# Performance work log

Measured on AMD Instinct MI355X. Metric: run time of the kernel, lower is better.

The kernel has to match this reference:

```python
import jax, jax.numpy as jnp
import numpy as np

N = 262144      # total line-graph nodes (16 graphs x 16384)
E = 2097152     # total line-graph edges (avg degree 8)
F_IN = 8        # edge_attr feature dim
FEATURES_DIM = 64


def gcn_conv(x, src, dst, W, b, n):
    """PyG GCNConv: x' = D^{-1/2} (A+I) D^{-1/2} (x W) + b, deg from in-edges incl. self-loops."""
    x = x @ W
    loop = jnp.arange(n, dtype=src.dtype)
    si = jnp.concatenate([src, loop])
    di = jnp.concatenate([dst, loop])
    deg = jax.ops.segment_sum(jnp.ones(si.shape[0], dtype=x.dtype), di, num_segments=n)
    dinv = jnp.where(deg > 0, deg ** -0.5, 0.0)
    norm = dinv[si] * dinv[di]                      # [E+N]
    msg = x[si] * norm[:, None]                     # gather + scale
    return jax.ops.segment_sum(msg, di, num_segments=n) + b


def setup_inputs() -> dict:
    key = jax.random.key(0)
    ks = jax.random.split(key, 10)

    def lin(k, fan_in, fan_out):
        return jax.random.normal(k, (fan_in, fan_out), jnp.float32) * (1.0 / np.sqrt(fan_in))

    return {
        "x": jax.random.normal(ks[0], (N, F_IN), jnp.float32),
        "W1": lin(ks[1], F_IN, 16), "b1": jnp.zeros((16,), jnp.float32),
        "W2": lin(ks[2], 16, 32),   "b2": jnp.zeros((32,), jnp.float32),
        "W3": lin(ks[3], 32, 64),   "b3": jnp.zeros((64,), jnp.float32),
        "Wfc": lin(ks[4], 64, FEATURES_DIM), "bfc": jnp.zeros((FEATURES_DIM,), jnp.float32),
        "edge_index": jax.random.randint(ks[5], (2, E), 0, N, dtype=jnp.int32),
        "batch_size": 16,
    }


def reference(x, W1, b1, W2, b2, W3, b3, Wfc, bfc, edge_index, batch_size):
    src, dst = edge_index[0], edge_index[1]
    n = x.shape[0]
    h = jax.nn.relu(gcn_conv(x, src, dst, W1, b1, n))
    h = jax.nn.relu(gcn_conv(h, src, dst, W2, b2, n))
    h = jax.nn.relu(gcn_conv(h, src, dst, W3, b3, n))
    out = h @ Wfc + bfc
    return out.reshape(batch_size, -1, FEATURES_DIM)
```

## Files before the change

kernel.cpp:

```cpp
#include <hip/hip_runtime.h>
#include <hip/hip_bf16.h>


#define NB   256
#define NPB  1024
#define TILE 4096
#define SRCMASK 0x3FFFFu

typedef _Float16 half8 __attribute__((ext_vector_type(8)));
typedef float float4v __attribute__((ext_vector_type(4)));

__device__ __forceinline__ unsigned pkh(float a, float b) {
    unsigned short ua = __builtin_bit_cast(unsigned short, (_Float16)a);
    unsigned short ub = __builtin_bit_cast(unsigned short, (_Float16)b);
    return (unsigned)ua | ((unsigned)ub << 16);
}
__device__ __forceinline__ float h_lo(unsigned u) {
    return (float)__builtin_bit_cast(_Float16, (unsigned short)(u & 0xFFFFu));
}
__device__ __forceinline__ float h_hi(unsigned u) {
    return (float)__builtin_bit_cast(_Float16, (unsigned short)(u >> 16));
}

__global__ void hist_kernel(const int* __restrict__ dst, int* __restrict__ ghist,
                            int E, int shift) {
    __shared__ int h[NB];
    int tid = threadIdx.x;
    h[tid] = 0;
    __syncthreads();
    int base = blockIdx.x * TILE;
    int cnt = min(TILE, E - base);
    for (int i = tid; i < cnt; i += 256)
        atomicAdd(&h[dst[base + i] >> shift], 1);
    __syncthreads();
    int v = h[tid];
    if (v) atomicAdd(&ghist[tid], v);
}

__global__ void bscan_kernel(const int* __restrict__ ghist, int* __restrict__ bbase,
                             int* __restrict__ gcursor,
                             const float* __restrict__ W3, const float* __restrict__ Wf,
                             _Float16* __restrict__ w3f, _Float16* __restrict__ wff) {
    __shared__ int sh[NB];
    int tid = threadIdx.x;
    int v = ghist[tid];
    sh[tid] = v;
    __syncthreads();
    for (int o = 1; o < NB; o <<= 1) {
        int t = (tid >= o) ? sh[tid - o] : 0;
        __syncthreads();
        sh[tid] += t;
        __syncthreads();
    }
    int incl = sh[tid];
    bbase[tid] = incl - v;
    gcursor[tid] = incl - v;
    if (tid == NB - 1) bbase[NB] = incl;
    for (int i = tid; i < 32 * 64; i += NB) {
        int k = i >> 6, j = i & 63;
        w3f[(j >> 4) * 512 + (j & 15) * 32 + (k >> 3) * 8 + (k & 7)] = (_Float16)W3[i];
    }
    for (int i = tid; i < 64 * 64; i += NB) {
        int k = i >> 6, j = i & 63;
        wff[((k >> 5) * 4 + (j >> 4)) * 512 + (j & 15) * 32 + ((k >> 3) & 3) * 8 + (k & 7)]
            = (_Float16)Wf[i];
    }
}

__global__ void __launch_bounds__(256)
partition_kernel(const int* __restrict__ src, const int* __restrict__ dst,
                 int* __restrict__ gcursor, unsigned int* __restrict__ bedge,
                 int E, int shift, int mask) {
    __shared__ int h[NB], st[NB], gp[NB];
    __shared__ unsigned short rk[TILE];
    __shared__ int sd[TILE];
    __shared__ int ss[TILE];
    int tid = threadIdx.x;
    h[tid] = 0;
    __syncthreads();
    int base = blockIdx.x * TILE;
    int cnt = min(TILE, E - base);
    for (int i = tid; i < cnt; i += 256)
        rk[i] = (unsigned short)atomicAdd(&h[dst[base + i] >> shift], 1);
    __syncthreads();
    int hv = h[tid];
    st[tid] = hv;
    __syncthreads();
    for (int o = 1; o < NB; o <<= 1) {
        int t = (tid >= o) ? st[tid - o] : 0;
        __syncthreads();
        st[tid] += t;
        __syncthreads();
    }
    st[tid] -= hv;
    gp[tid] = hv ? atomicAdd(&gcursor[tid], hv) : 0;
    __syncthreads();
    for (int i = tid; i < cnt; i += 256) {
        int d = dst[base + i];
        int b = d >> shift;
        int pos = st[b] + rk[i];
        sd[pos] = d;
        ss[pos] = src[base + i];
    }
    __syncthreads();
    for (int i = tid; i < cnt; i += 256) {
        int d = sd[i];
        int b = d >> shift;
        int g = gp[b] + (i - st[b]);
        bedge[g] = (unsigned int)ss[i] | ((unsigned int)(d & mask) << 18);
    }
}

__global__ void __launch_bounds__(256)
build_kernel(const int* __restrict__ bbase, const unsigned int* __restrict__ bedge,
             const float* __restrict__ x,
             int* __restrict__ off, float* __restrict__ dinv, int* __restrict__ adj,
             _Float16* __restrict__ y0h) {
    __shared__ int deg1[NPB];
    __shared__ int cur[NPB];
    __shared__ int bs[256];
    int tid = threadIdx.x;
    int b = blockIdx.x;
    int s = bbase[b], e = bbase[b + 1];
    int base = tid * 4;
#pragma unroll
    for (int i = 0; i < 4; i++) deg1[base + i] = 0;
    __syncthreads();
    for (int i = s + tid; i < e; i += 256)
        atomicAdd(&deg1[bedge[i] >> 18], 1);
    __syncthreads();
    int d0 = deg1[base], d1 = deg1[base + 1], d2 = deg1[base + 2], d3 = deg1[base + 3];
    int th = d0 + d1 + d2 + d3;
    bs[tid] = th;
    __syncthreads();
    for (int o = 1; o < 256; o <<= 1) {
        int t = (tid >= o) ? bs[tid - o] : 0;
        __syncthreads();
        bs[tid] += t;
        __syncthreads();
    }
    int run = s + bs[tid] - th;
    int vb = b * NPB + base;
    off[vb]     = run; cur[base]     = run; dinv[vb]     = rsqrtf((float)(d0 + 1)); run += d0;
    off[vb + 1] = run; cur[base + 1] = run; dinv[vb + 1] = rsqrtf((float)(d1 + 1)); run += d1;
    off[vb + 2] = run; cur[base + 2] = run; dinv[vb + 2] = rsqrtf((float)(d2 + 1)); run += d2;
    off[vb + 3] = run; cur[base + 3] = run; dinv[vb + 3] = rsqrtf((float)(d3 + 1)); run += d3;
    if (b == NB - 1 && tid == 255) off[NB * NPB] = e;
    __syncthreads();
    for (int i = s + tid; i < e; i += 256) {
        unsigned int pk = bedge[i];
        int p = atomicAdd(&cur[pk >> 18], 1);
        adj[p] = (int)(pk & SRCMASK);
    }
    for (int i = tid; i < NPB; i += 256) {
        float dv = rsqrtf((float)(deg1[i] + 1));
        const float4* xr = (const float4*)x + (size_t)(b * NPB + i) * 2;
        float4 t0 = xr[0], t1 = xr[1];
        uint4 pk;
        pk.x = pkh(t0.x * dv, t0.y * dv); pk.y = pkh(t0.z * dv, t0.w * dv);
        pk.z = pkh(t1.x * dv, t1.y * dv); pk.w = pkh(t1.z * dv, t1.w * dv);
        ((uint4*)y0h)[(size_t)b * NPB + i] = pk;
    }
}

__global__ void __launch_bounds__(256)
aggt1_kernel(const _Float16* __restrict__ y0h, const int* __restrict__ off,
             const int* __restrict__ adj, const float* __restrict__ dinv,
             const float* __restrict__ W1, const float* __restrict__ b1,
             _Float16* __restrict__ y1h) {
    __shared__ float Ws[8 * 16];
    __shared__ float bsh[16];
    __shared__ float sh[128][9];
    const int tid = threadIdx.x;
    if (tid < 128) Ws[tid] = W1[tid];
    if (tid < 16) bsh[tid] = b1[tid];
    const int vbase = blockIdx.x * 128;
    const int vl = tid >> 1, c = tid & 1;
    const int vg = vbase + vl;
    const uint2* y2 = (const uint2*)y0h;
    int beg = off[vg];
    int end = off[vg + 1];
    uint2 us = y2[(size_t)vg * 2 + c];
    float a0x = h_lo(us.x), a0y = h_hi(us.x), a0z = h_lo(us.y), a0w = h_hi(us.y);
    float a1x = 0, a1y = 0, a1z = 0, a1w = 0;
    float a2x = 0, a2y = 0, a2z = 0, a2w = 0;
    float a3x = 0, a3y = 0, a3z = 0, a3w = 0;
    int e = beg;
    for (; e + 4 <= end; e += 4) {
        int s0 = adj[e], s1 = adj[e + 1], s2 = adj[e + 2], s3 = adj[e + 3];
        uint2 u0 = y2[(size_t)s0 * 2 + c];
        uint2 u1 = y2[(size_t)s1 * 2 + c];
        uint2 u2 = y2[(size_t)s2 * 2 + c];
        uint2 u3 = y2[(size_t)s3 * 2 + c];
        a0x += h_lo(u0.x); a0y += h_hi(u0.x); a0z += h_lo(u0.y); a0w += h_hi(u0.y);
        a1x += h_lo(u1.x); a1y += h_hi(u1.x); a1z += h_lo(u1.y); a1w += h_hi(u1.y);
        a2x += h_lo(u2.x); a2y += h_hi(u2.x); a2z += h_lo(u2.y); a2w += h_hi(u2.y);
        a3x += h_lo(u3.x); a3y += h_hi(u3.x); a3z += h_lo(u3.y); a3w += h_hi(u3.y);
    }
    for (; e < end; e++) {
        uint2 u0 = y2[(size_t)adj[e] * 2 + c];
        a1x += h_lo(u0.x); a1y += h_hi(u0.x); a1z += h_lo(u0.y); a1w += h_hi(u0.y);
    }
    float dv = dinv[vg];
    sh[vl][c * 4 + 0] = ((a0x + a1x) + (a2x + a3x)) * dv;
    sh[vl][c * 4 + 1] = ((a0y + a1y) + (a2y + a3y)) * dv;
    sh[vl][c * 4 + 2] = ((a0z + a1z) + (a2z + a3z)) * dv;
    sh[vl][c * 4 + 3] = ((a0w + a1w) + (a2w + a3w)) * dv;
    __syncthreads();
    const int nl = tid & 127, hf = tid >> 7, j0 = hf * 8;
    float in0 = sh[nl][0], in1 = sh[nl][1], in2 = sh[nl][2], in3 = sh[nl][3];
    float in4 = sh[nl][4], in5 = sh[nl][5], in6 = sh[nl][6], in7 = sh[nl][7];
    float dn = dinv[vbase + nl];
    float o[8];
#pragma unroll
    for (int jj = 0; jj < 8; jj++) {
        int j = j0 + jj;
        float acc = bsh[j];
        acc += in0 * Ws[0 * 16 + j]; acc += in1 * Ws[1 * 16 + j];
        acc += in2 * Ws[2 * 16 + j]; acc += in3 * Ws[3 * 16 + j];
        acc += in4 * Ws[4 * 16 + j]; acc += in5 * Ws[5 * 16 + j];
        acc += in6 * Ws[6 * 16 + j]; acc += in7 * Ws[7 * 16 + j];
        o[jj] = dn * fmaxf(acc, 0.f);
    }
    uint4 pk;
    pk.x = pkh(o[0], o[1]); pk.y = pkh(o[2], o[3]);
    pk.z = pkh(o[4], o[5]); pk.w = pkh(o[6], o[7]);
    ((uint4*)y1h)[(size_t)(vbase + nl) * 2 + hf] = pk;
}

__global__ void __launch_bounds__(256)
aggt2_kernel(const _Float16* __restrict__ y1h, const int* __restrict__ off,
             const int* __restrict__ adj, const float* __restrict__ dinv,
             const float* __restrict__ W2, const float* __restrict__ b2,
             unsigned int* __restrict__ y2b) {
    __shared__ float Ws[16 * 32];
    __shared__ float bsh[32];
    __shared__ float sh[64][17];
    const int tid = threadIdx.x;
    for (int i = tid; i < 16 * 32; i += 256) Ws[i] = W2[i];
    if (tid < 32) bsh[tid] = b2[tid];
    const int vbase = blockIdx.x * 64;
    const int vl = tid >> 2, c = tid & 3;
    const int vg = vbase + vl;
    const uint2* y2 = (const uint2*)y1h;
    int beg = off[vg];
    int end = off[vg + 1];
    uint2 us = y2[(size_t)vg * 4 + c];
    float a0x = h_lo(us.x), a0y = h_hi(us.x), a0z = h_lo(us.y), a0w = h_hi(us.y);
    float a1x = 0, a1y = 0, a1z = 0, a1w = 0;
    float a2x = 0, a2y = 0, a2z = 0, a2w = 0;
    float a3x = 0, a3y = 0, a3z = 0, a3w = 0;
    int e = beg;
    for (; e + 4 <= end; e += 4) {
        int s0 = adj[e], s1 = adj[e + 1], s2 = adj[e + 2], s3 = adj[e + 3];
        uint2 u0 = y2[(size_t)s0 * 4 + c];
        uint2 u1 = y2[(size_t)s1 * 4 + c];
        uint2 u2 = y2[(size_t)s2 * 4 + c];
        uint2 u3 = y2[(size_t)s3 * 4 + c];
        a0x += h_lo(u0.x); a0y += h_hi(u0.x); a0z += h_lo(u0.y); a0w += h_hi(u0.y);
        a1x += h_lo(u1.x); a1y += h_hi(u1.x); a1z += h_lo(u1.y); a1w += h_hi(u1.y);
        a2x += h_lo(u2.x); a2y += h_hi(u2.x); a2z += h_lo(u2.y); a2w += h_hi(u2.y);
        a3x += h_lo(u3.x); a3y += h_hi(u3.x); a3z += h_lo(u3.y); a3w += h_hi(u3.y);
    }
    for (; e < end; e++) {
        uint2 u0 = y2[(size_t)adj[e] * 4 + c];
        a1x += h_lo(u0.x); a1y += h_hi(u0.x); a1z += h_lo(u0.y); a1w += h_hi(u0.y);
    }
    float dv = dinv[vg];
    sh[vl][c * 4 + 0] = ((a0x + a1x) + (a2x + a3x)) * dv;
    sh[vl][c * 4 + 1] = ((a0y + a1y) + (a2y + a3y)) * dv;
    sh[vl][c * 4 + 2] = ((a0z + a1z) + (a2z + a3z)) * dv;
    sh[vl][c * 4 + 3] = ((a0w + a1w) + (a2w + a3w)) * dv;
    __syncthreads();
    const int nl = tid & 63, q = tid >> 6, j0 = q * 8;
    float in[16];
#pragma unroll
    for (int k = 0; k < 16; k++) in[k] = sh[nl][k];
    float dn = dinv[vbase + nl];
    float o[8];
#pragma unroll
    for (int jj = 0; jj < 8; jj++) {
        int j = j0 + jj;
        float acc = bsh[j];
#pragma unroll
        for (int k = 0; k < 16; k++) acc += in[k] * Ws[k * 32 + j];
        o[jj] = dn * fmaxf(acc, 0.f);
    }
    uint4 pk;
    pk.x = pkh(o[0], o[1]); pk.y = pkh(o[2], o[3]);
    pk.z = pkh(o[4], o[5]); pk.w = pkh(o[6], o[7]);
    ((uint4*)y2b)[(size_t)(vbase + nl) * 4 + q] = pk;
}

__global__ void __launch_bounds__(256)
agg3_kernel(const unsigned int* __restrict__ y2b, const int* __restrict__ off,
            const int* __restrict__ adj, const float* __restrict__ dinv,
            _Float16* __restrict__ a3out, int n) {
    int t = blockIdx.x * 256 + threadIdx.x;
    int v = t >> 2, c = t & 3;
    if (v >= n) return;
    const uint4* yb = (const uint4*)y2b;
    uint4 us = yb[(size_t)v * 4 + c];
    float p0 = h_lo(us.x), p1 = h_hi(us.x), p2 = h_lo(us.y), p3 = h_hi(us.y);
    float p4 = h_lo(us.z), p5 = h_hi(us.z), p6 = h_lo(us.w), p7 = h_hi(us.w);
    float q0 = 0, q1 = 0, q2 = 0, q3 = 0, q4 = 0, q5 = 0, q6 = 0, q7 = 0;
    int beg = off[v], end = off[v + 1];
    int e = beg;
    for (; e + 2 <= end; e += 2) {
        int s0 = adj[e], s1 = adj[e + 1];
        uint4 u0 = yb[(size_t)s0 * 4 + c];
        uint4 u1 = yb[(size_t)s1 * 4 + c];
        p0 += h_lo(u0.x); p1 += h_hi(u0.x); p2 += h_lo(u0.y); p3 += h_hi(u0.y);
        p4 += h_lo(u0.z); p5 += h_hi(u0.z); p6 += h_lo(u0.w); p7 += h_hi(u0.w);
        q0 += h_lo(u1.x); q1 += h_hi(u1.x); q2 += h_lo(u1.y); q3 += h_hi(u1.y);
        q4 += h_lo(u1.z); q5 += h_hi(u1.z); q6 += h_lo(u1.w); q7 += h_hi(u1.w);
    }
    if (e < end) {
        uint4 u0 = yb[(size_t)adj[e] * 4 + c];
        p0 += h_lo(u0.x); p1 += h_hi(u0.x); p2 += h_lo(u0.y); p3 += h_hi(u0.y);
        p4 += h_lo(u0.z); p5 += h_hi(u0.z); p6 += h_lo(u0.w); p7 += h_hi(u0.w);
    }
    float dv = dinv[v];
    uint4 st;
    st.x = pkh((p0 + q0) * dv, (p1 + q1) * dv);
    st.y = pkh((p2 + q2) * dv, (p3 + q3) * dv);
    st.z = pkh((p4 + q4) * dv, (p5 + q5) * dv);
    st.w = pkh((p6 + q6) * dv, (p7 + q7) * dv);
    ((uint4*)a3out)[(size_t)v * 4 + c] = st;
}

__global__ void __launch_bounds__(256)
t3fc_kernel(const _Float16* __restrict__ a3h,
            const _Float16* __restrict__ w3f, const float* __restrict__ b3,
            const _Float16* __restrict__ wff, const float* __restrict__ bf,
            float* __restrict__ out) {
    __shared__ __align__(16) _Float16 tA[4][1024];
    const int tid = threadIdx.x;
    const int w = tid >> 6, l = tid & 63;
    const int lr = l & 15, lh = l >> 4;
    const int vbase = blockIdx.x * 64 + w * 16;
    const int fragoff = lr * 32 + lh * 8;

    half8 A1 = *(const half8*)(a3h + (size_t)(vbase + lr) * 32 + lh * 8);

    float4v c1[4];
#pragma unroll
    for (int nt = 0; nt < 4; nt++) {
        float bv = b3[nt * 16 + lr];
        float4v ci = {bv, bv, bv, bv};
        half8 B = *(const half8*)(w3f + nt * 512 + fragoff);
        c1[nt] = __builtin_amdgcn_mfma_f32_16x16x32_f16(A1, B, ci, 0, 0, 0);
    }

    _Float16* tw = tA[w];
#pragma unroll
    for (int nt = 0; nt < 4; nt++) {
        int k2 = nt * 16 + lr;
        int base = (k2 >> 5) * 512 + ((k2 >> 3) & 3) * 8 + (k2 & 7);
#pragma unroll
        for (int r = 0; r < 4; r++)
            tw[base + (lh * 4 + r) * 32] = (_Float16)fmaxf(c1[nt][r], 0.f);
    }

    float4v c2[4];
#pragma unroll
    for (int nt = 0; nt < 4; nt++) {
        float bv = bf[nt * 16 + lr];
        c2[nt] = (float4v){bv, bv, bv, bv};
    }
#pragma unroll
    for (int ks = 0; ks < 2; ks++) {
        half8 A2 = *(const half8*)(tw + ks * 512 + fragoff);
#pragma unroll
        for (int nt = 0; nt < 4; nt++) {
            half8 B = *(const half8*)(wff + (ks * 4 + nt) * 512 + fragoff);
            c2[nt] = __builtin_amdgcn_mfma_f32_16x16x32_f16(A2, B, c2[nt], 0, 0, 0);
        }
    }

#pragma unroll
    for (int nt = 0; nt < 4; nt++) {
#pragma unroll
        for (int r = 0; r < 4; r++)
            out[(size_t)(vbase + lh * 4 + r) * 64 + nt * 16 + lr] = c2[nt][r];
    }
}

extern "C" void kernel_launch(void* const* d_in, const int* in_sizes, int n_in,
                              void* d_out, int out_size, void* d_ws, size_t ws_size,
                              hipStream_t stream) {
    const float* x  = (const float*)d_in[0];
    const float* W1 = (const float*)d_in[1];
    const float* b1 = (const float*)d_in[2];
    const float* W2 = (const float*)d_in[3];
    const float* b2 = (const float*)d_in[4];
    const float* W3 = (const float*)d_in[5];
    const float* b3 = (const float*)d_in[6];
    const float* Wf = (const float*)d_in[7];
    const float* bf = (const float*)d_in[8];
    const int*   ei = (const int*)d_in[9];

    const int N = in_sizes[0] / 8;
    const int E = in_sizes[9] / 2;
    const int* srcv = ei;
    const int* dstv = ei + E;
    const int shift = 10;

    char* p = (char*)d_ws;
    auto take = [&p](size_t bytes) { char* q = p; p += (bytes + 63) & ~size_t(63); return q; };
    int*   off   = (int*)take((size_t)(N + 16) * 4);
    float* dinv  = (float*)take((size_t)N * 4);
    int*   adj   = (int*)take((size_t)E * 4);
    int*   ghist = (int*)take(NB * 4);
    int*   bbase = (int*)take((NB + 1) * 4);
    int*   gcur  = (int*)take(NB * 4);
    _Float16* w3f = (_Float16*)take(32 * 64 * 2);
    _Float16* wff = (_Float16*)take(64 * 64 * 2);
    char*  bufA  = take((size_t)N * 32 * 4);
    char*  bufB  = take((size_t)N * 16 * 4);
    char*  regX  = take((size_t)N * 32 * 2);
    unsigned int* bedge = (unsigned int*)regX;
    unsigned int* y2b   = (unsigned int*)regX;
    _Float16* y0h = (_Float16*)bufA;
    _Float16* a3h = (_Float16*)bufA;
    _Float16* y1h = (_Float16*)bufB;

    hipMemsetAsync(ghist, 0, NB * 4, stream);

    int nt = (E + TILE - 1) / TILE;
    hist_kernel<<<nt, 256, 0, stream>>>(dstv, ghist, E, shift);
    bscan_kernel<<<1, NB, 0, stream>>>(ghist, bbase, gcur, W3, Wf, w3f, wff);
    partition_kernel<<<nt, 256, 0, stream>>>(srcv, dstv, gcur, bedge, E, shift, NPB - 1);
    build_kernel<<<NB, 256, 0, stream>>>(bbase, bedge, x, off, dinv, adj, y0h);

    aggt1_kernel<<<N / 128, 256, 0, stream>>>(y0h, off, adj, dinv, W1, b1, y1h);
    aggt2_kernel<<<N / 64, 256, 0, stream>>>(y1h, off, adj, dinv, W2, b2, y2b);
    agg3_kernel<<<(N * 4) / 256, 256, 0, stream>>>(y2b, off, adj, dinv, a3h, N);
    t3fc_kernel<<<N / 64, 256, 0, stream>>>(a3h, w3f, b3, wff, bf, (float*)d_out);
}
```

Before: 290.4 us.

## Widen per-thread gathers to 16B and drop LDS staging in aggregation kernels

```diff
diff --git a/kernel.cpp b/kernel.cpp
--- a/kernel.cpp
+++ b/kernel.cpp
@@ -21,6 +21,10 @@
 __device__ __forceinline__ float h_hi(unsigned u) {
     return (float)__builtin_bit_cast(_Float16, (unsigned short)(u >> 16));
 }
+
+#define UNPK8_ADD(A, u) \
+    A##0 += h_lo(u.x); A##1 += h_hi(u.x); A##2 += h_lo(u.y); A##3 += h_hi(u.y); \
+    A##4 += h_lo(u.z); A##5 += h_hi(u.z); A##6 += h_lo(u.w); A##7 += h_hi(u.w);
 
 __global__ void hist_kernel(const int* __restrict__ dst, int* __restrict__ ghist,
                             int E, int shift) {
@@ -170,62 +174,77 @@
              _Float16* __restrict__ y1h) {
     __shared__ float Ws[8 * 16];
     __shared__ float bsh[16];
-    __shared__ float sh[128][9];
     const int tid = threadIdx.x;
     if (tid < 128) Ws[tid] = W1[tid];
     if (tid < 16) bsh[tid] = b1[tid];
-    const int vbase = blockIdx.x * 128;
-    const int vl = tid >> 1, c = tid & 1;
-    const int vg = vbase + vl;
-    const uint2* y2 = (const uint2*)y0h;
-    int beg = off[vg];
-    int end = off[vg + 1];
-    uint2 us = y2[(size_t)vg * 2 + c];
-    float a0x = h_lo(us.x), a0y = h_hi(us.x), a0z = h_lo(us.y), a0w = h_hi(us.y);
-    float a1x = 0, a1y = 0, a1z = 0, a1w = 0;
-    float a2x = 0, a2y = 0, a2z = 0, a2w = 0;
-    float a3x = 0, a3y = 0, a3z = 0, a3w = 0;
+    const int vg = blockIdx.x * 256 + tid;
+    const uint4* y4 = (const uint4*)y0h;
+    int beg = off[vg], end = off[vg + 1];
+    uint4 us = y4[vg];
+    float a0 = h_lo(us.x), a1 = h_hi(us.x), a2 = h_lo(us.y), a3 = h_hi(us.y),
+          a4 = h_lo(us.z), a5 = h_hi(us.z), a6 = h_lo(us.w), a7 = h_hi(us.w);
+    float c0 = 0, c1 = 0, c2 = 0, c3 = 0, c4 = 0, c5 = 0, c6 = 0, c7 = 0;
     int e = beg;
-    for (; e + 4 <= end; e += 4) {
+    for (; e + 8 <= end; e += 8) {
         int s0 = adj[e], s1 = adj[e + 1], s2 = adj[e + 2], s3 = adj[e + 3];
-        uint2 u0 = y2[(size_t)s0 * 2 + c];
-        uint2 u1 = y2[(size_t)s1 * 2 + c];
-        uint2 u2 = y2[(size_t)s2 * 2 + c];
-        uint2 u3 = y2[(size_t)s3 * 2 + c];
-        a0x += h_lo(u0.x); a0y += h_hi(u0.x); a0z += h_lo(u0.y); a0w += h_hi(u0.y);
-        a1x += h_lo(u1.x); a1y += h_hi(u1.x); a1z += h_lo(u1.y); a1w += h_hi(u1.y);
-        a2x += h_lo(u2.x); a2y += h_hi(u2.x); a2z += h_lo(u2.y); a2w += h_hi(u2.y);
-        a3x += h_lo(u3.x); a3y += h_hi(u3.x); a3z += h_lo(u3.y); a3w += h_hi(u3.y);
-    }
-    for (; e < end; e++) {
-        uint2 u0 = y2[(size_t)adj[e] * 2 + c];
-        a1x += h_lo(u0.x); a1y += h_hi(u0.x); a1z += h_lo(u0.y); a1w += h_hi(u0.y);
+        int s4 = adj[e + 4], s5 = adj[e + 5], s6 = adj[e + 6], s7 = adj[e + 7];
+        uint4 u0 = y4[s0], u1 = y4[s1], u2 = y4[s2], u3 = y4[s3];
+        uint4 u4 = y4[s4], u5 = y4[s5], u6 = y4[s6], u7 = y4[s7];
+        UNPK8_ADD(a, u0) UNPK8_ADD(c, u1) UNPK8_ADD(a, u2) UNPK8_ADD(c, u3)
+        UNPK8_ADD(a, u4) UNPK8_ADD(c, u5) UNPK8_ADD(a, u6) UNPK8_ADD(c, u7)
+    }
+    for (; e + 2 <= end; e += 2) {
+        int s0 = adj[e], s1 = adj[e + 1];
+        uint4 u0 = y4[s0], u1 = y4[s1];
+        UNPK8_ADD(a, u0) UNPK8_ADD(c, u1)
+    }
+    if (e < end) {
+        uint4 u0 = y4[adj[e]];
+        UNPK8_ADD(a, u0)
     }
     float dv = dinv[vg];
-    sh[vl][c * 4 + 0] = ((a0x + a1x) + (a2x + a3x)) * dv;
-    sh[vl][c * 4 + 1] = ((a0y + a1y) + (a2y + a3y)) * dv;
-    sh[vl][c * 4 + 2] = ((a0z + a1z) + (a2z + a3z)) * dv;
-    sh[vl][c * 4 + 3] = ((a0w + a1w) + (a2w + a3w)) * dv;
-    __syncthreads();
-    const int nl = tid & 127, hf = tid >> 7, j0 = hf * 8;
-    float in0 = sh[nl][0], in1 = sh[nl][1], in2 = sh[nl][2], in3 = sh[nl][3];
-    float in4 = sh[nl][4], in5 = sh[nl][5], in6 = sh[nl][6], in7 = sh[nl][7];
-    float dn = dinv[vbase + nl];
-    float o[8];
-#pragma unroll
-    for (int jj = 0; jj < 8; jj++) {
-        int j = j0 + jj;
-        float acc = bsh[j];
-        acc += in0 * Ws[0 * 16 + j]; acc += in1 * Ws[1 * 16 + j];
-        acc += in2 * Ws[2 * 16 + j]; acc += in3 * Ws[3 * 16 + j];
-        acc += in4 * Ws[4 * 16 + j]; acc += in5 * Ws[5 * 16 + j];
-        acc += in6 * Ws[6 * 16 + j]; acc += in7 * Ws[7 * 16 + j];
-        o[jj] = dn * fmaxf(acc, 0.f);
-    }
-    uint4 pk;
-    pk.x = pkh(o[0], o[1]); pk.y = pkh(o[2], o[3]);
-    pk.z = pkh(o[4], o[5]); pk.w = pkh(o[6], o[7]);
-    ((uint4*)y1h)[(size_t)(vbase + nl) * 2 + hf] = pk;
+    float in[8];
+    in[0] = (a0 + c0) * dv; in[1] = (a1 + c1) * dv;
+    in[2] = (a2 + c2) * dv; in[3] = (a3 + c3) * dv;
+    in[4] = (a4 + c4) * dv; in[5] = (a5 + c5) * dv;
+    in[6] = (a6 + c6) * dv; in[7] = (a7 + c7) * dv;
+    __syncthreads();
+    const float4* W4 = (const float4*)Ws;
+    float o[16];
+    {
+        float4 b0 = ((const float4*)bsh)[0], b1v = ((const float4*)bsh)[1];
+        float4 b2v = ((const float4*)bsh)[2], b3v = ((const float4*)bsh)[3];
+        o[0] = b0.x; o[1] = b0.y; o[2] = b0.z; o[3] = b0.w;
+        o[4] = b1v.x; o[5] = b1v.y; o[6] = b1v.z; o[7] = b1v.w;
+        o[8] = b2v.x; o[9] = b2v.y; o[10] = b2v.z; o[11] = b2v.w;
+        o[12] = b3v.x; o[13] = b3v.y; o[14] = b3v.z; o[15] = b3v.w;
+    }
+#pragma unroll
+    for (int k = 0; k < 8; k++) {
+        float xk = in[k];
+        float4 w0 = W4[k * 4 + 0], w1 = W4[k * 4 + 1];
+        float4 w2 = W4[k * 4 + 2], w3 = W4[k * 4 + 3];
+        o[0] = fmaf(xk, w0.x, o[0]);  o[1] = fmaf(xk, w0.y, o[1]);
+        o[2] = fmaf(xk, w0.z, o[2]);  o[3] = fmaf(xk, w0.w, o[3]);
+        o[4] = fmaf(xk, w1.x, o[4]);  o[5] = fmaf(xk, w1.y, o[5]);
+        o[6] = fmaf(xk, w1.z, o[6]);  o[7] = fmaf(xk, w1.w, o[7]);
+        o[8] = fmaf(xk, w2.x, o[8]);  o[9] = fmaf(xk, w2.y, o[9]);
+        o[10] = fmaf(xk, w2.z, o[10]); o[11] = fmaf(xk, w2.w, o[11]);
+        o[12] = fmaf(xk, w3.x, o[12]); o[13] = fmaf(xk, w3.y, o[13]);
+        o[14] = fmaf(xk, w3.z, o[14]); o[15] = fmaf(xk, w3.w, o[15]);
+    }
+    uint4 p0, p1;
+    p0.x = pkh(dv * fmaxf(o[0], 0.f),  dv * fmaxf(o[1], 0.f));
+    p0.y = pkh(dv * fmaxf(o[2], 0.f),  dv * fmaxf(o[3], 0.f));
+    p0.z = pkh(dv * fmaxf(o[4], 0.f),  dv * fmaxf(o[5], 0.f));
+    p0.w = pkh(dv * fmaxf(o[6], 0.f),  dv * fmaxf(o[7], 0.f));
+    p1.x = pkh(dv * fmaxf(o[8], 0.f),  dv * fmaxf(o[9], 0.f));
+    p1.y = pkh(dv * fmaxf(o[10], 0.f), dv * fmaxf(o[11], 0.f));
+    p1.z = pkh(dv * fmaxf(o[12], 0.f), dv * fmaxf(o[13], 0.f));
+    p1.w = pkh(dv * fmaxf(o[14], 0.f), dv * fmaxf(o[15], 0.f));
+    uint4* out4 = (uint4*)y1h;
+    out4[(size_t)vg * 2]     = p0;
+    out4[(size_t)vg * 2 + 1] = p1;
 }
 
 __global__ void __launch_bounds__(256)
@@ -235,61 +254,88 @@
              unsigned int* __restrict__ y2b) {
     __shared__ float Ws[16 * 32];
     __shared__ float bsh[32];
-    __shared__ float sh[64][17];
     const int tid = threadIdx.x;
     for (int i = tid; i < 16 * 32; i += 256) Ws[i] = W2[i];
     if (tid < 32) bsh[tid] = b2[tid];
-    const int vbase = blockIdx.x * 64;
-    const int vl = tid >> 2, c = tid & 3;
+    const int vbase = blockIdx.x * 128;
+    const int vl = tid >> 1, c = tid & 1;
     const int vg = vbase + vl;
-    const uint2* y2 = (const uint2*)y1h;
-    int beg = off[vg];
-    int end = off[vg + 1];
-    uint2 us = y2[(size_t)vg * 4 + c];
-    float a0x = h_lo(us.x), a0y = h_hi(us.x), a0z = h_lo(us.y), a0w = h_hi(us.y);
-    float a1x = 0, a1y = 0, a1z = 0, a1w = 0;
-    float a2x = 0, a2y = 0, a2z = 0, a2w = 0;
-    float a3x = 0, a3y = 0, a3z = 0, a3w = 0;
+    const uint4* y4 = (const uint4*)y1h;
+    int beg = off[vg], end = off[vg + 1];
+    uint4 us = y4[(size_t)vg * 2 + c];
+    float a0 = h_lo(us.x), a1 = h_hi(us.x), a2 = h_lo(us.y), a3 = h_hi(us.y),
+          a4 = h_lo(us.z), a5 = h_hi(us.z), a6 = h_lo(us.w), a7 = h_hi(us.w);
+    float c0 = 0, c1 = 0, c2 = 0, c3 = 0, c4 = 0, c5 = 0, c6 = 0, c7 = 0;
     int e = beg;
-    for (; e + 4 <= end; e += 4) {
+    for (; e + 8 <= end; e += 8) {
         int s0 = adj[e], s1 = adj[e + 1], s2 = adj[e + 2], s3 = adj[e + 3];
-        uint2 u0 = y2[(size_t)s0 * 4 + c];
-        uint2 u1 = y2[(size_t)s1 * 4 + c];
-        uint2 u2 = y2[(size_t)s2 * 4 + c];
-        uint2 u3 = y2[(size_t)s3 * 4 + c];
-        a0x += h_lo(u0.x); a0y += h_hi(u0.x); a0z += h_lo(u0.y); a0w += h_hi(u0.y);
-        a1x += h_lo(u1.x); a1y += h_hi(u1.x); a1z += h_lo(u1.y); a1w += h_hi(u1.y);
-        a2x += h_lo(u2.x); a2y += h_hi(u2.x); a2z += h_lo(u2.y); a2w += h_hi(u2.y);
-        a3x += h_lo(u3.x); a3y += h_hi(u3.x); a3z += h_lo(u3.y); a3w += h_hi(u3.y);
-    }
-    for (; e < end; e++) {
-        uint2 u0 = y2[(size_t)adj[e] * 4 + c];
-        a1x += h_lo(u0.x); a1y += h_hi(u0.x); a1z += h_lo(u0.y); a1w += h_hi(u0.y);
+        int s4 = adj[e + 4], s5 = adj[e + 5], s6 = adj[e + 6], s7 = adj[e + 7];
+        uint4 u0 = y4[(size_t)s0 * 2 + c], u1 = y4[(size_t)s1 * 2 + c];
+        uint4 u2 = y4[(size_t)s2 * 2 + c], u3 = y4[(size_t)s3 * 2 + c];
+        uint4 u4 = y4[(size_t)s4 * 2 + c], u5 = y4[(size_t)s5 * 2 + c];
+        uint4 u6 = y4[(size_t)s6 * 2 + c], u7 = y4[(size_t)s7 * 2 + c];
+        UNPK8_ADD(a, u0) UNPK8_ADD(c, u1) UNPK8_ADD(a, u2) UNPK8_ADD(c, u3)
+        UNPK8_ADD(a, u4) UNPK8_ADD(c, u5) UNPK8_ADD(a, u6) UNPK8_ADD(c, u7)
+    }
+    for (; e + 2 <= end; e += 2) {
+        int s0 = adj[e], s1 = adj[e + 1];
+        uint4 u0 = y4[(size_t)s0 * 2 + c], u1 = y4[(size_t)s1 * 2 + c];
+        UNPK8_ADD(a, u0) UNPK8_ADD(c, u1)
+    }
+    if (e < end) {
+        uint4 u0 = y4[(size_t)adj[e] * 2 + c];
+        UNPK8_ADD(a, u0)
     }
     float dv = dinv[vg];
-    sh[vl][c * 4 + 0] = ((a0x + a1x) + (a2x + a3x)) * dv;
-    sh[vl][c * 4 + 1] = ((a0y + a1y) + (a2y + a3y)) * dv;
-    sh[vl][c * 4 + 2] = ((a0z + a1z) + (a2z + a3z)) * dv;
-    sh[vl][c * 4 + 3] = ((a0w + a1w) + (a2w + a3w)) * dv;
-    __syncthreads();
-    const int nl = tid & 63, q = tid >> 6, j0 = q * 8;
+    float own[8];
+    own[0] = (a0 + c0) * dv; own[1] = (a1 + c1) * dv;
+    own[2] = (a2 + c2) * dv; own[3] = (a3 + c3) * dv;
+    own[4] = (a4 + c4) * dv; own[5] = (a5 + c5) * dv;
+    own[6] = (a6 + c6) * dv; own[7] = (a7 + c7) * dv;
+    float oth[8];
+#pragma unroll
+    for (int k = 0; k < 8; k++) oth[k] = __shfl_xor(own[k], 1);
     float in[16];
 #pragma unroll
-    for (int k = 0; k < 16; k++) in[k] = sh[nl][k];
-    float dn = dinv[vbase + nl];
-    float o[8];
-#pragma unroll
-    for (int jj = 0; jj < 8; jj++) {
-        int j = j0 + jj;
-        float acc = bsh[j];
-#pragma unroll
-        for (int k = 0; k < 16; k++) acc += in[k] * Ws[k * 32 + j];
-        o[jj] = dn * fmaxf(acc, 0.f);
-    }
-    uint4 pk;
-    pk.x = pkh(o[0], o[1]); pk.y = pkh(o[2], o[3]);
-    pk.z = pkh(o[4], o[5]); pk.w = pkh(o[6], o[7]);
-    ((uint4*)y2b)[(size_t)(vbase + nl) * 4 + q] = pk;
+    for (int k = 0; k < 8; k++) {
+        in[c * 8 + k] = own[k];
+        in[(1 - c) * 8 + k] = oth[k];
+    }
+    __syncthreads();
+    const int j0 = c * 16;
+    const float4* W4 = (const float4*)Ws;
+    float o[16];
+#pragma unroll
+    for (int jj = 0; jj < 16; jj += 4) {
+        float4 bv = *(const float4*)&bsh[j0 + jj];
+        o[jj] = bv.x; o[jj + 1] = bv.y; o[jj + 2] = bv.z; o[jj + 3] = bv.w;
+    }
+#pragma unroll
+    for (int k = 0; k < 16; k++) {
+        float xk = in[k];
+        float4 w0 = W4[k * 8 + c * 4 + 0], w1 = W4[k * 8 + c * 4 + 1];
+        float4 w2 = W4[k * 8 + c * 4 + 2], w3 = W4[k * 8 + c * 4 + 3];
+        o[0] = fmaf(xk, w0.x, o[0]);  o[1] = fmaf(xk, w0.y, o[1]);
+        o[2] = fmaf(xk, w0.z, o[2]);  o[3] = fmaf(xk, w0.w, o[3]);
+        o[4] = fmaf(xk, w1.x, o[4]);  o[5] = fmaf(xk, w1.y, o[5]);
+        o[6] = fmaf(xk, w1.z, o[6]);  o[7] = fmaf(xk, w1.w, o[7]);
+        o[8] = fmaf(xk, w2.x, o[8]);  o[9] = fmaf(xk, w2.y, o[9]);
+        o[10] = fmaf(xk, w2.z, o[10]); o[11] = fmaf(xk, w2.w, o[11]);
+        o[12] = fmaf(xk, w3.x, o[12]); o[13] = fmaf(xk, w3.y, o[13]);
+        o[14] = fmaf(xk, w3.z, o[14]); o[15] = fmaf(xk, w3.w, o[15]);
+    }
+    uint4 p0, p1;
+    p0.x = pkh(dv * fmaxf(o[0], 0.f),  dv * fmaxf(o[1], 0.f));
+    p0.y = pkh(dv * fmaxf(o[2], 0.f),  dv * fmaxf(o[3], 0.f));
+    p0.z = pkh(dv * fmaxf(o[4], 0.f),  dv * fmaxf(o[5], 0.f));
+    p0.w = pkh(dv * fmaxf(o[6], 0.f),  dv * fmaxf(o[7], 0.f));
+    p1.x = pkh(dv * fmaxf(o[8], 0.f),  dv * fmaxf(o[9], 0.f));
+    p1.y = pkh(dv * fmaxf(o[10], 0.f), dv * fmaxf(o[11], 0.f));
+    p1.z = pkh(dv * fmaxf(o[12], 0.f), dv * fmaxf(o[13], 0.f));
+    p1.w = pkh(dv * fmaxf(o[14], 0.f), dv * fmaxf(o[15], 0.f));
+    uint4* out4 = (uint4*)y2b;
+    out4[(size_t)vg * 4 + c * 2]     = p0;
+    out4[(size_t)vg * 4 + c * 2 + 1] = p1;
 }
 
 __global__ void __launch_bounds__(256)
@@ -301,31 +347,35 @@
     if (v >= n) return;
     const uint4* yb = (const uint4*)y2b;
     uint4 us = yb[(size_t)v * 4 + c];
-    float p0 = h_lo(us.x), p1 = h_hi(us.x), p2 = h_lo(us.y), p3 = h_hi(us.y);
-    float p4 = h_lo(us.z), p5 = h_hi(us.z), p6 = h_lo(us.w), p7 = h_hi(us.w);
-    float q0 = 0, q1 = 0, q2 = 0, q3 = 0, q4 = 0, q5 = 0, q6 = 0, q7 = 0;
+    float a0 = h_lo(us.x), a1 = h_hi(us.x), a2 = h_lo(us.y), a3 = h_hi(us.y),
+          a4 = h_lo(us.z), a5 = h_hi(us.z), a6 = h_lo(us.w), a7 = h_hi(us.w);
+    float c0 = 0, c1 = 0, c2 = 0, c3 = 0, c4 = 0, c5 = 0, c6 = 0, c7 = 0;
     int beg = off[v], end = off[v + 1];
     int e = beg;
+    for (; e + 4 <= end; e += 4) {
+        int s0 = adj[e], s1 = adj[e + 1], s2 = adj[e + 2], s3 = adj[e + 3];
+        uint4 u0 = yb[(size_t)s0 * 4 + c];
+        uint4 u1 = yb[(size_t)s1 * 4 + c];
+        uint4 u2 = yb[(size_t)s2 * 4 + c];
+        uint4 u3 = yb[(size_t)s3 * 4 + c];
+        UNPK8_ADD(a, u0) UNPK8_ADD(c, u1) UNPK8_ADD(a, u2) UNPK8_ADD(c, u3)
+    }
     for (; e + 2 <= end; e += 2) {
         int s0 = adj[e], s1 = adj[e + 1];
         uint4 u0 = yb[(size_t)s0 * 4 + c];
         uint4 u1 = yb[(size_t)s1 * 4 + c];
-        p0 += h_lo(u0.x); p1 += h_hi(u0.x); p2 += h_lo(u0.y); p3 += h_hi(u0.y);
-        p4 += h_lo(u0.z); p5 += h_hi(u0.z); p6 += h_lo(u0.w); p7 += h_hi(u0.w);
-        q0 += h_lo(u1.x); q1 += h_hi(u1.x); q2 += h_lo(u1.y); q3 += h_hi(u1.y);
-        q4 += h_lo(u1.z); q5 += h_hi(u1.z); q6 += h_lo(u1.w); q7 += h_hi(u1.w);
+        UNPK8_ADD(a, u0) UNPK8_ADD(c, u1)
     }
     if (e < end) {
         uint4 u0 = yb[(size_t)adj[e] * 4 + c];
-        p0 += h_lo(u0.x); p1 += h_hi(u0.x); p2 += h_lo(u0.y); p3 += h_hi(u0.y);
-        p4 += h_lo(u0.z); p5 += h_hi(u0.z); p6 += h_lo(u0.w); p7 += h_hi(u0.w);
+        UNPK8_ADD(a, u0)
     }
     float dv = dinv[v];
     uint4 st;
-    st.x = pkh((p0 + q0) * dv, (p1 + q1) * dv);
-    st.y = pkh((p2 + q2) * dv, (p3 + q3) * dv);
-    st.z = pkh((p4 + q4) * dv, (p5 + q5) * dv);
-    st.w = pkh((p6 + q6) * dv, (p7 + q7) * dv);
+    st.x = pkh((a0 + c0) * dv, (a1 + c1) * dv);
+    st.y = pkh((a2 + c2) * dv, (a3 + c3) * dv);
+    st.z = pkh((a4 + c4) * dv, (a5 + c5) * dv);
+    st.w = pkh((a6 + c6) * dv, (a7 + c7) * dv);
     ((uint4*)a3out)[(size_t)v * 4 + c] = st;
 }
 
@@ -433,8 +483,8 @@
     partition_kernel<<<nt, 256, 0, stream>>>(srcv, dstv, gcur, bedge, E, shift, NPB - 1);
     build_kernel<<<NB, 256, 0, stream>>>(bbase, bedge, x, off, dinv, adj, y0h);
 
-    aggt1_kernel<<<N / 128, 256, 0, stream>>>(y0h, off, adj, dinv, W1, b1, y1h);
-    aggt2_kernel<<<N / 64, 256, 0, stream>>>(y1h, off, adj, dinv, W2, b2, y2b);
+    aggt1_kernel<<<N / 256, 256, 0, stream>>>(y0h, off, adj, dinv, W1, b1, y1h);
+    aggt2_kernel<<<N / 128, 256, 0, stream>>>(y1h, off, adj, dinv, W2, b2, y2b);
     agg3_kernel<<<(N * 4) / 256, 256, 0, stream>>>(y2b, off, adj, dinv, a3h, N);
     t3fc_kernel<<<N / 64, 256, 0, stream>>>(a3h, w3f, b3, wff, bf, (float*)d_out);
 }
```

Measured after the change: 283.0 us. 2.5% less time.
